# Optimization experiments

Hardware: AMD Instinct MI355X
Metric: run time of the kernel (lower is better)

The kernel has to match this reference:

```python
import jax, jax.numpy as jnp
import numpy as np

B, S = 4, 16384
D_IN, D_HID, D_KEY, D_VAL, N_HEADS = 512, 2048, 64, 64, 8
SEG_FULL, SAMP = 2048, 4
SEG = SEG_FULL // SAMP  # 512: MoD capacity per segment, also attn segment_len


def setup_inputs() -> dict:
    key = jax.random.key(0)
    ks = jax.random.split(key, 10)
    sc = lambda i, shape: (jax.random.normal(ks[i], shape, jnp.float32) * 0.02)
    return {
        "x": jax.random.normal(ks[0], (B, S, D_IN), jnp.float32),
        "w_samp": sc(1, (D_IN, 1)), "b_samp": jnp.zeros((1,), jnp.float32),
        "w_q": sc(2, (D_IN, N_HEADS * D_KEY)),
        "w_k": sc(3, (D_IN, N_HEADS * D_KEY)),
        "w_v": sc(4, (D_IN, N_HEADS * D_VAL)),
        "w_o": sc(5, (N_HEADS * D_VAL, D_IN)),
        "betas": jax.random.normal(ks[6], (1, N_HEADS, 1, D_VAL), jnp.float32),
        "w1": sc(7, (D_IN, D_HID)), "b1": jnp.zeros((D_HID,), jnp.float32),
        "w2": sc(8, (D_HID, D_IN)), "b2": jnp.zeros((D_IN,), jnp.float32),
    }


def _cm_attention(x, w_q, w_k, w_v, w_o, betas):
    """CompressiveMemory: segment-recurrent linear-attn memory + local softmax attn."""
    b, n, _ = x.shape
    nseg = n // SEG

    def split(w, dh):
        y = (x @ w).reshape(b, n, N_HEADS, dh).transpose(0, 2, 1, 3)          # [b,H,n,dh]
        return y.reshape(b, N_HEADS, nseg, SEG, dh).transpose(2, 0, 1, 3, 4)  # [nseg,b,H,SEG,dh]

    qs, ks_, vs = split(w_q, D_KEY), split(w_k, D_KEY), split(w_v, D_VAL)
    gate = jax.nn.sigmoid(betas)                                              # [1,H,1,dv]
    mem0 = jnp.zeros((b, N_HEADS, D_KEY, D_VAL), x.dtype)
    z0 = jnp.ones((b, N_HEADS, D_KEY, 1), x.dtype) / D_KEY
    scale = D_KEY ** -0.5

    def step(carry, seg):
        mem, z = carry
        q, k, v = seg
        sq = jax.nn.elu(q) + 1.0
        sk = jax.nn.elu(k) + 1.0
        scores = jnp.einsum('bhqk,bhsk->bhqs', q, k) * scale
        att_dot = jax.nn.softmax(scores, axis=-1) @ v                         # [b,H,SEG,dv]
        att_mem = (sq @ mem) / (sq @ z)                                       # uses pre-update mem,z
        mem = mem + jnp.einsum('bhsk,bhsv->bhkv', sk, v)                      # linear update
        z = z + sk.sum(axis=-2)[..., None]
        att = gate * att_mem + (1.0 - gate) * att_dot
        return (mem, z), att

    _, outs = jax.lax.scan(step, (mem0, z0), (qs, ks_, vs))                   # [nseg,b,H,SEG,dv]
    out = outs.transpose(1, 0, 3, 2, 4).reshape(b, n, N_HEADS * D_VAL)
    return out @ w_o


def reference(x, w_samp, b_samp, w_q, w_k, w_v, w_o, betas, w1, b1, w2, b2):
    b, s, d = x.shape
    nseg = s // SEG_FULL
    scores = (x @ w_samp + b_samp)[..., 0]                                    # [B,S]
    # top-SEG tokens per full segment (training-mode routing), kept in sequence order
    seg_scores = scores.reshape(b, nseg, SEG_FULL)
    top = jnp.argsort(-seg_scores, axis=-1)[:, :, :SEG]                       # [B,nseg,SEG]
    sel = jnp.sort(top, axis=-1) + (jnp.arange(nseg) * SEG_FULL)[None, :, None]
    flat = sel.reshape(b, nseg * SEG)                                         # global indices, [B,Ssel]
    x_sel = jnp.take_along_axis(x, flat[..., None], axis=1)                   # gather [B,Ssel,D]
    h = _cm_attention(x_sel, w_q, w_k, w_v, w_o, betas)
    h = jax.nn.gelu(h @ w1 + b1, approximate=False) @ w2 + b2                 # MLP (dropout=0)
    bi = jnp.arange(b)[:, None]
    x_out = x.at[bi, flat].add(h)                                             # scatter-add back
    mask = jnp.zeros((b, s), x.dtype).at[bi, flat].set(1.0)
    # faithful to source: zero positions >= number of selected tokens
    pad = (jnp.arange(s)[None, :] < mask.sum(axis=1)[:, None]).astype(x.dtype)
    x_out = x_out * pad[..., None]
    return x_out, mask.reshape(-1, 1), scores.reshape(-1, 1)
```

## Files before the change

kernel.cpp:

```cpp
#include <hip/hip_runtime.h>
#include <math.h>

#define S_TOT 16384
#define BATCH 4
#define DIN 512
#define NH 8
#define DK 64
#define SEGF 2048
#define SEGS 512
#define NSEG 8
#define NUSE 2
#define MROWS (BATCH*NUSE*SEGS)

typedef unsigned int u32;
typedef __attribute__((ext_vector_type(8))) short short8;
typedef __attribute__((ext_vector_type(4))) float f32x4;

__device__ __forceinline__ short f2b(float f) {
  u32 u = __float_as_uint(f);
  u32 r = u + 0x7fffu + ((u >> 16) & 1u);
  return (short)(r >> 16);
}
__device__ __forceinline__ float b2f(short s) {
  return __uint_as_float(((u32)(unsigned short)s) << 16);
}

__global__ __launch_bounds__(256) void scores_transpose(
    const float* __restrict__ x, const float* __restrict__ w,
    const float* __restrict__ bsamp, float* __restrict__ out,
    const float* __restrict__ w_q, const float* __restrict__ w_k,
    const float* __restrict__ w_v, const float* __restrict__ w_o,
    const float* __restrict__ w1,  const float* __restrict__ w2,
    short* __restrict__ Wtqkv, short* __restrict__ Wto,
    short* __restrict__ Wt1,   short* __restrict__ Wt2)
{
  __shared__ float t[32][33];
  int tid = threadIdx.x;
  if (blockIdx.x < 16384) {
    int tok  = blockIdx.x * 4 + (tid >> 6);
    int lane = tid & 63;
    const float4* xr = (const float4*)(x + (size_t)tok * DIN);
    const float4* wr = (const float4*)w;
    float4 a0 = xr[lane],      w0 = wr[lane];
    float4 a1 = xr[lane + 64], w1v = wr[lane + 64];
    float p = a0.x*w0.x + a0.y*w0.y + a0.z*w0.z + a0.w*w0.w
            + a1.x*w1v.x + a1.y*w1v.y + a1.z*w1v.z + a1.w*w1v.w;
    #pragma unroll
    for (int off = 32; off > 0; off >>= 1) p += __shfl_down(p, off);
    if (lane == 0) out[tok] = p + bsamp[0];
    return;
  }
  int bid = blockIdx.x - 16384;
  const float* src; short* dst; int K, N, rowoff, tIdx;
  if (bid < 1024) {
    K = 512; N = 512; tIdx = bid & 255;
    int which = bid >> 8;
    src = which == 0 ? w_q : which == 1 ? w_k : which == 2 ? w_v : w_o;
    dst = which == 3 ? Wto : Wtqkv;
    rowoff = which == 3 ? 0 : which * 512;
  } else if (bid < 2048) {
    K = 512; N = 2048; tIdx = bid - 1024; src = w1; dst = Wt1; rowoff = 0;
  } else {
    K = 2048; N = 512; tIdx = bid - 2048; src = w2; dst = Wt2; rowoff = 0;
  }
  int ntN = N >> 5;
  int n0 = (tIdx % ntN) * 32, k0 = (tIdx / ntN) * 32;
  int txx = tid & 31, ty = tid >> 5;
  #pragma unroll
  for (int r = 0; r < 4; ++r)
    t[ty + 8*r][txx] = src[(size_t)(k0 + ty + 8*r) * N + n0 + txx];
  __syncthreads();
  #pragma unroll
  for (int r = 0; r < 4; ++r)
    dst[(size_t)(rowoff + n0 + ty + 8*r) * K + k0 + txx] = f2b(t[txx][ty + 8*r]);
}

__global__ __launch_bounds__(256) void topk_rank(
    const float* __restrict__ scores, int* __restrict__ flags,
    float* __restrict__ maskOut)
{
  int c = blockIdx.x & 7, g = (blockIdx.x >> 3) & 7, b = blockIdx.x >> 6;
  __shared__ float sc[SEGF];
  int tid = threadIdx.x;
  const float* src = scores + (size_t)b*S_TOT + (size_t)g*SEGF;
  *(float4*)&sc[tid*8]     = *(const float4*)(src + tid*8);
  *(float4*)&sc[tid*8 + 4] = *(const float4*)(src + tid*8 + 4);
  __syncthreads();
  int i0 = c*256 + tid;
  float mine = sc[i0];
  int cnt = 0;
  #pragma unroll 2
  for (int j = 0; j < SEGF; j += 8) {
    float4 a = *(const float4*)&sc[j];
    float4 d = *(const float4*)&sc[j + 4];
    cnt += (a.x > mine || (a.x == mine && (j+0) < i0)) ? 1 : 0;
    cnt += (a.y > mine || (a.y == mine && (j+1) < i0)) ? 1 : 0;
    cnt += (a.z > mine || (a.z == mine && (j+2) < i0)) ? 1 : 0;
    cnt += (a.w > mine || (a.w == mine && (j+3) < i0)) ? 1 : 0;
    cnt += (d.x > mine || (d.x == mine && (j+4) < i0)) ? 1 : 0;
    cnt += (d.y > mine || (d.y == mine && (j+5) < i0)) ? 1 : 0;
    cnt += (d.z > mine || (d.z == mine && (j+6) < i0)) ? 1 : 0;
    cnt += (d.w > mine || (d.w == mine && (j+7) < i0)) ? 1 : 0;
  }
  int flg = (cnt < SEGS) ? 1 : 0;
  flags[(((b << 3) + g) << 11) + i0] = flg;
  maskOut[(size_t)b*S_TOT + (size_t)g*SEGF + i0] = flg ? 1.0f : 0.0f;
}

__global__ __launch_bounds__(256) void topk_compact(
    const int* __restrict__ flags, int* __restrict__ flat, int* __restrict__ inv)
{
  int g = blockIdx.x & 1, b = blockIdx.x >> 1;
  __shared__ int wsum[4];
  int tid = threadIdx.x;
  int lane = tid & 63, w = tid >> 6;
  const int* f = flags + (((b << 3) + g) << 11);
  int fl[8]; int ls = 0;
  #pragma unroll
  for (int l = 0; l < 8; ++l) { fl[l] = f[tid*8 + l]; ls += fl[l]; }
  int inc = ls;
  #pragma unroll
  for (int off = 1; off < 64; off <<= 1) {
    int t = __shfl_up(inc, off);
    if (lane >= off) inc += t;
  }
  if (lane == 63) wsum[w] = inc;
  __syncthreads();
  int base = 0;
  #pragma unroll
  for (int ww = 0; ww < 4; ++ww) base += (ww < w) ? wsum[ww] : 0;
  int pos = base + inc - ls;
  #pragma unroll
  for (int l = 0; l < 8; ++l) {
    int i = tid*8 + l;
    inv[b*(NUSE*SEGF) + g*SEGF + i] = fl[l] ? (g*SEGS + pos) : -1;
    if (fl[l]) {
      flat[b*(NSEG*SEGS) + g*SEGS + pos] = g*SEGF + i;
      pos++;
    }
  }
}

__global__ __launch_bounds__(256) void gather_cast(
    const float* __restrict__ x, const int* __restrict__ flat,
    short* __restrict__ xsel)
{
  int tok  = blockIdx.x * 4 + (threadIdx.x >> 6);
  int lane = threadIdx.x & 63;
  int b = tok >> 10, i = tok & 1023;
  int gidx = flat[b * (NSEG*SEGS) + i];
  const float* srcp = x + ((size_t)(b * S_TOT + gidx)) * DIN + lane*8;
  float4 a0 = *(const float4*)srcp;
  float4 a1 = *(const float4*)(srcp + 4);
  uint4 o;
  o.x = (u32)(unsigned short)f2b(a0.x) | ((u32)(unsigned short)f2b(a0.y) << 16);
  o.y = (u32)(unsigned short)f2b(a0.z) | ((u32)(unsigned short)f2b(a0.w) << 16);
  o.z = (u32)(unsigned short)f2b(a1.x) | ((u32)(unsigned short)f2b(a1.y) << 16);
  o.w = (u32)(unsigned short)f2b(a1.z) | ((u32)(unsigned short)f2b(a1.w) << 16);
  *(uint4*)(xsel + (size_t)tok * DIN + lane*8) = o;
}

template<int BM, int BN, int WM, int WN>
__global__ __launch_bounds__(256) void gemm_bf16(
    const short* __restrict__ A, const short* __restrict__ Bt,
    const float* __restrict__ bias, float* __restrict__ Cf,
    short* __restrict__ Cb, short* __restrict__ VtOut, short* __restrict__ KtOut,
    int M, int N, int K, int act)
{
  constexpr int BK = 64;
  constexpr int WAVES_N = BN / WN;
  constexpr int FM = WM / 16, FN = WN / 16;
  __shared__ short Al[2][BM * BK];
  __shared__ short Bl[2][BN * BK];
  const int tid = threadIdx.x;
  const int lane = tid & 63, wid = tid >> 6;
  const int wr = wid / WAVES_N, wc = wid % WAVES_N;
  const int bm = blockIdx.y * BM, bn = blockIdx.x * BN;
  const int ln15 = lane & 15, hi8 = (lane >> 4) * 8;

  f32x4 acc[FM][FN];
  #pragma unroll
  for (int i = 0; i < FM; ++i)
    #pragma unroll
    for (int j = 0; j < FN; ++j)
      #pragma unroll
      for (int e = 0; e < 4; ++e) acc[i][j][e] = 0.f;

  const int NT = K / BK;

  auto stage = [&](int t, int buf) {
    const int k0 = t * BK;
    #pragma unroll
    for (int i = 0; i < BM/32; ++i) {
      int slot = i*256 + tid;
      int row = slot >> 3, col = (slot & 7) * 8;
      const short* gp = A + (size_t)(bm + row) * K + k0 + col;
      __builtin_amdgcn_global_load_lds(
          (const __attribute__((address_space(1))) void*)gp,
          (__attribute__((address_space(3))) void*)&Al[buf][row*BK + col],
          16, 0, 0);
    }
    #pragma unroll
    for (int i = 0; i < BN/32; ++i) {
      int slot = i*256 + tid;
      int row = slot >> 3, col = (slot & 7) * 8;
      const short* gp = Bt + (size_t)(bn + row) * K + k0 + col;
      __builtin_amdgcn_global_load_lds(
          (const __attribute__((address_space(1))) void*)gp,
          (__attribute__((address_space(3))) void*)&Bl[buf][row*BK + col],
          16, 0, 0);
    }
  };

  stage(0, 0);
  __syncthreads();
  int cur = 0;
  for (int t = 0; t < NT; ++t) {
    if (t + 1 < NT) stage(t + 1, cur ^ 1);
    #pragma unroll
    for (int ks = 0; ks < 2; ++ks) {
      short8 af[FM], bf_[FN];
      #pragma unroll
      for (int fm = 0; fm < FM; ++fm)
        af[fm] = *(const short8*)&Al[cur][(wr*WM + fm*16 + ln15)*BK + ks*32 + hi8];
      #pragma unroll
      for (int fn = 0; fn < FN; ++fn)
        bf_[fn] = *(const short8*)&Bl[cur][(wc*WN + fn*16 + ln15)*BK + ks*32 + hi8];
      #pragma unroll
      for (int fm = 0; fm < FM; ++fm)
        #pragma unroll
        for (int fn = 0; fn < FN; ++fn)
          acc[fm][fn] = __builtin_amdgcn_mfma_f32_16x16x32_bf16(af[fm], bf_[fn], acc[fm][fn], 0, 0, 0);
    }
    __syncthreads();
    cur ^= 1;
  }

  const int crow0 = (lane >> 4) * 4, ccol = lane & 15;
  #pragma unroll
  for (int fm = 0; fm < FM; ++fm) {
    #pragma unroll
    for (int fn = 0; fn < FN; ++fn) {
      int c = bn + wc*WN + fn*16 + ccol;
      int r0 = bm + wr*WM + fm*16 + crow0;
      float vv[4];
      #pragma unroll
      for (int j = 0; j < 4; ++j) {
        float v = acc[fm][fn][j];
        if (bias) v += bias[c];
        if (act == 1) v = 0.5f * v * (1.0f + erff(v * 0.70710678118f));
        vv[j] = v;
        if (Cf) Cf[(size_t)(r0 + j) * N + c] = v;
        if (Cb) Cb[(size_t)(r0 + j) * N + c] = f2b(v);
      }
      if (VtOut && c >= 1024) {
        int hh = (c - 1024) >> 6, dv = c & 63;
        int bb = r0 >> 10, key = r0 & 1023;
        u32 lo = (u32)(unsigned short)f2b(vv[0]) | ((u32)(unsigned short)f2b(vv[1]) << 16);
        u32 hi = (u32)(unsigned short)f2b(vv[2]) | ((u32)(unsigned short)f2b(vv[3]) << 16);
        *(uint2*)&VtOut[((size_t)((bb*8 + hh)*64 + dv) << 10) + key] = make_uint2(lo, hi);
      }
      if (KtOut && c >= 512 && c < 1024) {
        int hh = (c - 512) >> 6, dk = c & 63;
        int bb = r0 >> 10, key = r0 & 1023;
        float e0 = vv[0] > 0.f ? vv[0] + 1.f : __expf(vv[0]);
        float e1 = vv[1] > 0.f ? vv[1] + 1.f : __expf(vv[1]);
        float e2 = vv[2] > 0.f ? vv[2] + 1.f : __expf(vv[2]);
        float e3 = vv[3] > 0.f ? vv[3] + 1.f : __expf(vv[3]);
        u32 lo = (u32)(unsigned short)f2b(e0) | ((u32)(unsigned short)f2b(e1) << 16);
        u32 hi = (u32)(unsigned short)f2b(e2) | ((u32)(unsigned short)f2b(e3) << 16);
        *(uint2*)&KtOut[((size_t)((bb*8 + hh)*64 + dk) << 10) + key] = make_uint2(lo, hi);
      }
    }
  }
}

__global__ __launch_bounds__(256) void memsum_mfma(
    const short* __restrict__ Kt, const short* __restrict__ Vt,
    short* __restrict__ m0t, float* __restrict__ zf)
{
  int b = blockIdx.x >> 3, h = blockIdx.x & 7;
  const short* ktb = Kt + ((size_t)((b*8+h)*64) << 10);
  const short* vtb = Vt + ((size_t)((b*8+h)*64) << 10);
  int tid = threadIdx.x, lane = tid & 63, w = tid >> 6;
  int ln15 = lane & 15, hi8 = (lane >> 4) * 8;
  f32x4 acc[4];
  #pragma unroll
  for (int nf = 0; nf < 4; ++nf) acc[nf] = (f32x4){0.f,0.f,0.f,0.f};
  #pragma unroll 4
  for (int ks = 0; ks < 16; ++ks) {
    short8 a = *(const short8*)&vtb[(size_t)(w*16 + ln15)*1024 + ks*32 + hi8];
    #pragma unroll
    for (int nf = 0; nf < 4; ++nf) {
      short8 bfr = *(const short8*)&ktb[(size_t)(nf*16 + ln15)*1024 + ks*32 + hi8];
      acc[nf] = __builtin_amdgcn_mfma_f32_16x16x32_bf16(a, bfr, acc[nf], 0, 0, 0);
    }
  }
  size_t mb = (size_t)(b*NH + h) * 4096;
  #pragma unroll
  for (int nf = 0; nf < 4; ++nf)
    #pragma unroll
    for (int j = 0; j < 4; ++j)
      m0t[mb + (size_t)(w*16 + (lane>>4)*4 + j)*64 + nf*16 + ln15] = f2b(acc[nf][j]);
  int row = tid >> 2, q = tid & 3;
  float zs = 0.f;
  #pragma unroll 4
  for (int i = 0; i < 16; ++i) {
    short8 kv = *(const short8*)&ktb[(size_t)row*1024 + q*128 + i*8];
    #pragma unroll
    for (int e = 0; e < 8; ++e) zs += b2f(kv[e]);
  }
  zs += __shfl_xor(zs, 1); zs += __shfl_xor(zs, 2);
  if (q == 0) zf[(b*8+h)*64 + row] = 0.015625f + zs;
}

__global__ __launch_bounds__(256) void attn4(
    const short* __restrict__ qkv, const short* __restrict__ vt,
    const short* __restrict__ m0t, const float* __restrict__ zf,
    const float* __restrict__ betas, short* __restrict__ att)
{
  __shared__ short Ks[128*64];
  __shared__ short Vts[64*128];
  __shared__ short Ps[4*16*128];
  __shared__ float zl[64];
  __shared__ float relay[64];
  int tid = threadIdx.x, lane = tid & 63, w = tid >> 6;
  int ln15 = lane & 15, hi8 = (lane >> 4) * 8;
  int bx = blockIdx.x;
  int qt = bx & 7, h = (bx >> 3) & 7, g = (bx >> 6) & 1, b = bx >> 7;
  const int seg0 = b*1024 + g*512;
  const int qbase = seg0 + qt*64;

  short8 qf[2];
  {
    const short* qg = qkv + (size_t)(qbase + w*16 + ln15)*1536 + h*64;
    qf[0] = *(const short8*)(qg + hi8);
    qf[1] = *(const short8*)(qg + 32 + hi8);
  }
  if (g && tid < 16) *(float4*)&zl[tid*4] = *(const float4*)(zf + (size_t)(b*8+h)*64 + tid*4);

  const short* kg = qkv + (size_t)seg0*1536 + 512 + h*64;
  const short* vg = vt + ((size_t)((b*8+h)*64) << 10) + g*512;
  short* Pw = &Ps[w*2048];

  f32x4 oacc[4];
  #pragma unroll
  for (int nf = 0; nf < 4; ++nf) oacc[nf] = (f32x4){0.f,0.f,0.f,0.f};
  float lsum[4] = {0.f,0.f,0.f,0.f};

  for (int c = 0; c < 4; ++c) {
    __syncthreads();
    #pragma unroll
    for (int p = 0; p < 4; ++p) {
      int slot = p*256 + tid;
      int row = slot >> 3;
      int off = ((slot & 7)*8) ^ ((row & 7)*8);
      __builtin_amdgcn_global_load_lds(
        (const __attribute__((address_space(1))) void*)(kg + (size_t)(c*128 + row)*1536 + off),
        (__attribute__((address_space(3))) void*)&Ks[slot*8], 16, 0, 0);
    }
    #pragma unroll
    for (int p = 0; p < 4; ++p) {
      int slot = p*256 + tid;
      int row = slot >> 4;
      int off = ((slot & 15)*8) ^ ((row & 7)*8);
      __builtin_amdgcn_global_load_lds(
        (const __attribute__((address_space(1))) void*)(vg + ((size_t)row << 10) + c*128 + off),
        (__attribute__((address_space(3))) void*)&Vts[slot*8], 16, 0, 0);
    }
    __syncthreads();

    f32x4 sf[8];
    #pragma unroll
    for (int nf = 0; nf < 8; ++nf) sf[nf] = (f32x4){0.f,0.f,0.f,0.f};
    __builtin_amdgcn_s_setprio(1);
    #pragma unroll
    for (int ks = 0; ks < 2; ++ks)
      #pragma unroll
      for (int nf = 0; nf < 8; ++nf) {
        int row = nf*16 + ln15;
        short8 kb = *(const short8*)&Ks[row*64 + ((ks*32 + hi8) ^ ((row&7)*8))];
        sf[nf] = __builtin_amdgcn_mfma_f32_16x16x32_bf16(qf[ks], kb, sf[nf], 0, 0, 0);
      }
    __builtin_amdgcn_s_setprio(0);
    #pragma unroll
    for (int nf = 0; nf < 8; ++nf)
      #pragma unroll
      for (int j = 0; j < 4; ++j) {
        float p = __expf(sf[nf][j] * 0.125f);
        lsum[j] += p;
        int q = (lane >> 4)*4 + j;
        int key = nf*16 + ln15;
        Pw[q*128 + (key ^ ((q&7)*8))] = f2b(p);
      }
    __builtin_amdgcn_s_setprio(1);
    #pragma unroll
    for (int ks = 0; ks < 4; ++ks) {
      short8 pa = *(const short8*)&Pw[ln15*128 + ((ks*32 + hi8) ^ ((ln15&7)*8))];
      #pragma unroll
      for (int nf = 0; nf < 4; ++nf) {
        int row = nf*16 + ln15;
        short8 vb = *(const short8*)&Vts[row*128 + ((ks*32 + hi8) ^ ((row&7)*8))];
        oacc[nf] = __builtin_amdgcn_mfma_f32_16x16x32_bf16(pa, vb, oacc[nf], 0, 0, 0);
      }
    }
    __builtin_amdgcn_s_setprio(0);
  }

  float linv[4];
  #pragma unroll
  for (int j = 0; j < 4; ++j) {
    float s = lsum[j];
    s += __shfl_xor(s, 1); s += __shfl_xor(s, 2);
    s += __shfl_xor(s, 4); s += __shfl_xor(s, 8);
    linv[j] = 1.f / s;
  }

  f32x4 mfr[4];
  #pragma unroll
  for (int nf = 0; nf < 4; ++nf) mfr[nf] = (f32x4){0.f,0.f,0.f,0.f};
  float dinv[4] = {0.f,0.f,0.f,0.f};
  if (g) {
    __syncthreads();
    const short* mg = m0t + (size_t)(b*8+h)*4096;
    #pragma unroll
    for (int p = 0; p < 2; ++p) {
      int slot = p*256 + tid;
      int row = slot >> 3;
      int off = ((slot & 7)*8) ^ ((row & 7)*8);
      __builtin_amdgcn_global_load_lds(
        (const __attribute__((address_space(1))) void*)(mg + (size_t)row*64 + off),
        (__attribute__((address_space(3))) void*)&Ks[slot*8], 16, 0, 0);
    }
    __syncthreads();
    float sqv[2][8]; short8 sqf[2];
    #pragma unroll
    for (int ks = 0; ks < 2; ++ks)
      #pragma unroll
      for (int e = 0; e < 8; ++e) {
        float f = b2f(qf[ks][e]);
        f = f > 0.f ? f + 1.f : __expf(f);
        sqv[ks][e] = f; sqf[ks][e] = f2b(f);
      }
    float denp = 0.f;
    #pragma unroll
    for (int ks = 0; ks < 2; ++ks)
      #pragma unroll
      for (int e = 0; e < 8; ++e) denp += sqv[ks][e] * zl[ks*32 + hi8 + e];
    denp += __shfl_xor(denp, 16); denp += __shfl_xor(denp, 32);
    if (lane < 16) relay[w*16 + lane] = denp;
    #pragma unroll
    for (int ks = 0; ks < 2; ++ks)
      #pragma unroll
      for (int nf = 0; nf < 4; ++nf) {
        int row = nf*16 + ln15;
        short8 mb_ = *(const short8*)&Ks[row*64 + ((ks*32 + hi8) ^ ((row&7)*8))];
        mfr[nf] = __builtin_amdgcn_mfma_f32_16x16x32_bf16(sqf[ks], mb_, mfr[nf], 0, 0, 0);
      }
    #pragma unroll
    for (int j = 0; j < 4; ++j)
      dinv[j] = 1.f / relay[w*16 + (lane>>4)*4 + j];
  }

  #pragma unroll
  for (int nf = 0; nf < 4; ++nf) {
    float bt = betas[h*64 + nf*16 + ln15];
    float gt = 1.f / (1.f + __expf(-bt));
    #pragma unroll
    for (int j = 0; j < 4; ++j) {
      float ad = oacc[nf][j] * linv[j];
      float v = g ? (gt * mfr[nf][j] * dinv[j] + (1.f - gt) * ad) : (1.f - gt) * ad;
      int qrow = qbase + w*16 + (lane>>4)*4 + j;
      att[(size_t)qrow*512 + h*64 + nf*16 + ln15] = f2b(v);
    }
  }
}

__global__ __launch_bounds__(256) void final_kernel(
    const float* __restrict__ x, const int* __restrict__ inv,
    const float* __restrict__ hm, float* __restrict__ outX)
{
  int row  = blockIdx.x * 4 + (threadIdx.x >> 6);
  int lane = threadIdx.x & 63;
  int b = row >> 14;
  int s = row & (S_TOT - 1);
  size_t base = (size_t)row * DIN + lane * 8;
  if (s >= NUSE * SEGF) {
    float4 z = make_float4(0.f,0.f,0.f,0.f);
    *(float4*)(outX + base)     = z;
    *(float4*)(outX + base + 4) = z;
    return;
  }
  float4 a0 = *(const float4*)(x + base);
  float4 a1 = *(const float4*)(x + base + 4);
  int i = inv[b * (NUSE*SEGF) + s];
  if (i >= 0) {
    size_t hb = (size_t)(b * (NUSE*SEGS) + i) * DIN + lane * 8;
    float4 h0 = *(const float4*)(hm + hb);
    float4 h1 = *(const float4*)(hm + hb + 4);
    a0.x += h0.x; a0.y += h0.y; a0.z += h0.z; a0.w += h0.w;
    a1.x += h1.x; a1.y += h1.y; a1.z += h1.z; a1.w += h1.w;
  }
  *(float4*)(outX + base)     = a0;
  *(float4*)(outX + base + 4) = a1;
}

extern "C" void kernel_launch(void* const* d_in, const int* in_sizes, int n_in,
                              void* d_out, int out_size, void* d_ws, size_t ws_size,
                              hipStream_t stream) {
  (void)in_sizes; (void)n_in; (void)out_size; (void)ws_size;
  const float* x      = (const float*)d_in[0];
  const float* w_samp = (const float*)d_in[1];
  const float* b_samp = (const float*)d_in[2];
  const float* w_q    = (const float*)d_in[3];
  const float* w_k    = (const float*)d_in[4];
  const float* w_v    = (const float*)d_in[5];
  const float* w_o    = (const float*)d_in[6];
  const float* betas  = (const float*)d_in[7];
  const float* w1     = (const float*)d_in[8];
  const float* b1     = (const float*)d_in[9];
  const float* w2     = (const float*)d_in[10];
  const float* b2     = (const float*)d_in[11];

  float* outX      = (float*)d_out;
  float* outMask   = outX + (size_t)BATCH * S_TOT * DIN;
  float* outScores = outMask + (size_t)BATCH * S_TOT;

  char* ws = (char*)d_ws;
  int*   flat  = (int*)(ws);
  int*   inv   = (int*)(ws + 65536);
  int*   flags = (int*)(ws + 131072);
  short* M0t   = (short*)(ws + 393216);
  float* Zf    = (float*)(ws + 655360);
  short* Wtqkv = (short*)(ws + 1048576);
  short* Wto   = (short*)(ws + 2621440);
  short* Wt1   = (short*)(ws + 3145728);
  short* Wt2   = (short*)(ws + 5242880);
  short* xsel  = (short*)(ws + 7340032);
  short* qkv   = (short*)(ws + 11534336);
  short* Vt    = (short*)(ws + 24117248);
  short* attb  = (short*)(ws + 28311552);
  short* R0b   = (short*)(ws + 32505856);
  short* Kt    = (short*)(ws + 36700160);
  short* hidB  = (short*)(ws + 7340032);
  float* Hf    = (float*)(ws + 24117248);

  scores_transpose<<<16384 + 3072, 256, 0, stream>>>(
      x, w_samp, b_samp, outScores,
      w_q, w_k, w_v, w_o, w1, w2, Wtqkv, Wto, Wt1, Wt2);
  topk_rank<<<BATCH*NSEG*8, 256, 0, stream>>>(outScores, flags, outMask);
  topk_compact<<<BATCH*NUSE, 256, 0, stream>>>(flags, flat, inv);

  gather_cast<<<MROWS/4, 256, 0, stream>>>(x, flat, xsel);

  gemm_bf16<128,128,64,64><<<dim3(12,32), 256, 0, stream>>>(
      xsel, Wtqkv, nullptr, nullptr, qkv, Vt, Kt, MROWS, 1536, 512, 0);

  memsum_mfma<<<BATCH*NH, 256, 0, stream>>>(Kt, Vt, M0t, Zf);
  attn4<<<512, 256, 0, stream>>>(qkv, Vt, M0t, Zf, betas, attb);

  gemm_bf16<64,64,32,32><<<dim3(8,64), 256, 0, stream>>>(
      attb, Wto, nullptr, nullptr, R0b, nullptr, nullptr, MROWS, 512, 512, 0);
  gemm_bf16<128,128,64,64><<<dim3(16,32), 256, 0, stream>>>(
      R0b, Wt1, b1, nullptr, hidB, nullptr, nullptr, MROWS, 2048, 512, 1);
  gemm_bf16<64,64,32,32><<<dim3(8,64), 256, 0, stream>>>(
      hidB, Wt2, b2, Hf, nullptr, nullptr, nullptr, MROWS, 512, 2048, 0);

  final_kernel<<<(BATCH*S_TOT)/4, 256, 0, stream>>>(x, inv, Hf, outX);
}
```

Measured before the change: 248.7 us.

## Fold output projection into first MLP weight and make GEMM BK a template parameter

Precomputes the fused weight (w_o @ w1) with a small GEMM on the weights, so the attention output feeds the first MLP GEMM directly and the separate output-projection GEMM and its intermediate buffer are removed. w_o is now cast to bf16 without transposing, so it serves as the B-transposed operand for the fusion GEMM. The GEMM kernel gains a BK template parameter, and the large GEMMs switch to BK=32. Rounding the fused weight to bf16 changes numerics slightly, and a weight-sized GEMM is added on every call.

```diff
diff --git a/kernel.cpp b/kernel.cpp
--- a/kernel.cpp
+++ b/kernel.cpp
@@ -31,7 +31,7 @@
     const float* __restrict__ w_q, const float* __restrict__ w_k,
     const float* __restrict__ w_v, const float* __restrict__ w_o,
     const float* __restrict__ w1,  const float* __restrict__ w2,
-    short* __restrict__ Wtqkv, short* __restrict__ Wto,
+    short* __restrict__ Wtqkv, short* __restrict__ Wob,
     short* __restrict__ Wt1,   short* __restrict__ Wt2)
 {
   __shared__ float t[32][33];
@@ -51,13 +51,24 @@
     return;
   }
   int bid = blockIdx.x - 16384;
+  int txx = tid & 31, ty = tid >> 5;
+  if (bid >= 768 && bid < 1024) {
+    int tIdx = bid - 768;
+    int n0 = (tIdx & 15) * 32, k0 = (tIdx >> 4) * 32;
+    #pragma unroll
+    for (int r = 0; r < 4; ++r) {
+      size_t idx = (size_t)(k0 + ty + 8*r) * 512 + n0 + txx;
+      Wob[idx] = f2b(w_o[idx]);
+    }
+    return;
+  }
   const float* src; short* dst; int K, N, rowoff, tIdx;
-  if (bid < 1024) {
+  if (bid < 768) {
     K = 512; N = 512; tIdx = bid & 255;
     int which = bid >> 8;
-    src = which == 0 ? w_q : which == 1 ? w_k : which == 2 ? w_v : w_o;
-    dst = which == 3 ? Wto : Wtqkv;
-    rowoff = which == 3 ? 0 : which * 512;
+    src = which == 0 ? w_q : which == 1 ? w_k : w_v;
+    dst = Wtqkv;
+    rowoff = which * 512;
   } else if (bid < 2048) {
     K = 512; N = 2048; tIdx = bid - 1024; src = w1; dst = Wt1; rowoff = 0;
   } else {
@@ -65,7 +76,6 @@
   }
   int ntN = N >> 5;
   int n0 = (tIdx % ntN) * 32, k0 = (tIdx / ntN) * 32;
-  int txx = tid & 31, ty = tid >> 5;
   #pragma unroll
   for (int r = 0; r < 4; ++r)
     t[ty + 8*r][txx] = src[(size_t)(k0 + ty + 8*r) * N + n0 + txx];
@@ -160,16 +170,16 @@
   *(uint4*)(xsel + (size_t)tok * DIN + lane*8) = o;
 }
 
-template<int BM, int BN, int WM, int WN>
+template<int BM, int BN, int WM, int WN, int BK>
 __global__ __launch_bounds__(256) void gemm_bf16(
     const short* __restrict__ A, const short* __restrict__ Bt,
     const float* __restrict__ bias, float* __restrict__ Cf,
     short* __restrict__ Cb, short* __restrict__ VtOut, short* __restrict__ KtOut,
     int M, int N, int K, int act)
 {
-  constexpr int BK = 64;
   constexpr int WAVES_N = BN / WN;
   constexpr int FM = WM / 16, FN = WN / 16;
+  constexpr int RPB = BK / 8;
   __shared__ short Al[2][BM * BK];
   __shared__ short Bl[2][BN * BK];
   const int tid = threadIdx.x;
@@ -191,9 +201,9 @@
   auto stage = [&](int t, int buf) {
     const int k0 = t * BK;
     #pragma unroll
-    for (int i = 0; i < BM/32; ++i) {
+    for (int i = 0; i < BM*BK/2048; ++i) {
       int slot = i*256 + tid;
-      int row = slot >> 3, col = (slot & 7) * 8;
+      int row = slot / RPB, col = (slot % RPB) * 8;
       const short* gp = A + (size_t)(bm + row) * K + k0 + col;
       __builtin_amdgcn_global_load_lds(
           (const __attribute__((address_space(1))) void*)gp,
@@ -201,9 +211,9 @@
           16, 0, 0);
     }
     #pragma unroll
-    for (int i = 0; i < BN/32; ++i) {
+    for (int i = 0; i < BN*BK/2048; ++i) {
       int slot = i*256 + tid;
-      int row = slot >> 3, col = (slot & 7) * 8;
+      int row = slot / RPB, col = (slot % RPB) * 8;
       const short* gp = Bt + (size_t)(bn + row) * K + k0 + col;
       __builtin_amdgcn_global_load_lds(
           (const __attribute__((address_space(1))) void*)gp,
@@ -218,7 +228,7 @@
   for (int t = 0; t < NT; ++t) {
     if (t + 1 < NT) stage(t + 1, cur ^ 1);
     #pragma unroll
-    for (int ks = 0; ks < 2; ++ks) {
+    for (int ks = 0; ks < BK/32; ++ks) {
       short8 af[FM], bf_[FN];
       #pragma unroll
       for (int fm = 0; fm < FM; ++fm)
@@ -533,37 +543,38 @@
   short* M0t   = (short*)(ws + 393216);
   float* Zf    = (float*)(ws + 655360);
   short* Wtqkv = (short*)(ws + 1048576);
-  short* Wto   = (short*)(ws + 2621440);
+  short* Wob   = (short*)(ws + 2621440);
   short* Wt1   = (short*)(ws + 3145728);
   short* Wt2   = (short*)(ws + 5242880);
   short* xsel  = (short*)(ws + 7340032);
   short* qkv   = (short*)(ws + 11534336);
   short* Vt    = (short*)(ws + 24117248);
   short* attb  = (short*)(ws + 28311552);
-  short* R0b   = (short*)(ws + 32505856);
   short* Kt    = (short*)(ws + 36700160);
+  short* WfT   = (short*)(ws + 40894464);
   short* hidB  = (short*)(ws + 7340032);
   float* Hf    = (float*)(ws + 24117248);
 
   scores_transpose<<<16384 + 3072, 256, 0, stream>>>(
       x, w_samp, b_samp, outScores,
-      w_q, w_k, w_v, w_o, w1, w2, Wtqkv, Wto, Wt1, Wt2);
+      w_q, w_k, w_v, w_o, w1, w2, Wtqkv, Wob, Wt1, Wt2);
   topk_rank<<<BATCH*NSEG*8, 256, 0, stream>>>(outScores, flags, outMask);
   topk_compact<<<BATCH*NUSE, 256, 0, stream>>>(flags, flat, inv);
 
+  gemm_bf16<64,64,32,32,64><<<dim3(8,32), 256, 0, stream>>>(
+      Wt1, Wob, nullptr, nullptr, WfT, nullptr, nullptr, 2048, 512, 512, 0);
+
   gather_cast<<<MROWS/4, 256, 0, stream>>>(x, flat, xsel);
 
-  gemm_bf16<128,128,64,64><<<dim3(12,32), 256, 0, stream>>>(
+  gemm_bf16<128,128,64,64,32><<<dim3(12,32), 256, 0, stream>>>(
       xsel, Wtqkv, nullptr, nullptr, qkv, Vt, Kt, MROWS, 1536, 512, 0);
 
   memsum_mfma<<<BATCH*NH, 256, 0, stream>>>(Kt, Vt, M0t, Zf);
   attn4<<<512, 256, 0, stream>>>(qkv, Vt, M0t, Zf, betas, attb);
 
-  gemm_bf16<64,64,32,32><<<dim3(8,64), 256, 0, stream>>>(
-      attb, Wto, nullptr, nullptr, R0b, nullptr, nullptr, MROWS, 512, 512, 0);
-  gemm_bf16<128,128,64,64><<<dim3(16,32), 256, 0, stream>>>(
-      R0b, Wt1, b1, nullptr, hidB, nullptr, nullptr, MROWS, 2048, 512, 1);
-  gemm_bf16<64,64,32,32><<<dim3(8,64), 256, 0, stream>>>(
+  gemm_bf16<128,128,64,64,32><<<dim3(16,32), 256, 0, stream>>>(
+      attb, WfT, b1, nullptr, hidB, nullptr, nullptr, MROWS, 2048, 512, 1);
+  gemm_bf16<64,64,32,32,64><<<dim3(8,64), 256, 0, stream>>>(
       hidB, Wt2, b2, Hf, nullptr, nullptr, nullptr, MROWS, 512, 2048, 0);
 
   final_kernel<<<(BATCH*S_TOT)/4, 256, 0, stream>>>(x, inv, Hf, outX);
```

After: 245.9 us. Within noise of the previous version (-1.2%).
